# Performance work log

Measured on AMD Instinct MI355X. Metric: run time of the kernel, lower is better.

The kernel has to match this reference:

```python
import jax, jax.numpy as jnp
import numpy as np

D_MODEL = 512
NUM_HEADS = 8
D_K = D_MODEL // NUM_HEADS


def setup_inputs() -> dict:
    key = jax.random.key(0)
    ks = jax.random.split(key, 11)
    B, S = 2, 4096
    s = 1.0 / np.sqrt(D_MODEL)
    inp = {
        "q": jax.random.normal(ks[0], (B, S, D_MODEL), jnp.float32),
        "k": jax.random.normal(ks[1], (B, S, D_MODEL), jnp.float32),
        "v": jax.random.normal(ks[2], (B, S, D_MODEL), jnp.float32),
        "W_q": jax.random.normal(ks[3], (D_MODEL, D_MODEL), jnp.float32) * s,
        "b_q": jnp.zeros((D_MODEL,), jnp.float32),
        "W_k": jax.random.normal(ks[4], (D_MODEL, D_MODEL), jnp.float32) * s,
        "b_k": jnp.zeros((D_MODEL,), jnp.float32),
        "W_v": jax.random.normal(ks[5], (D_MODEL, D_MODEL), jnp.float32) * s,
        "b_v": jnp.zeros((D_MODEL,), jnp.float32),
        "W_o": jax.random.normal(ks[6], (D_MODEL, D_MODEL), jnp.float32) * s,
        "b_o": jnp.zeros((D_MODEL,), jnp.float32),
    }
    return inp


def reference(q, k, v, W_q, b_q, W_k, b_k, W_v, b_v, W_o, b_o):
    B, S, _ = q.shape

    def proj(x, W, b):
        # Linear then split heads: [B,S,D] -> [B,H,S,d_k]
        y = x @ W.T + b
        return y.reshape(B, S, NUM_HEADS, D_K).transpose(0, 2, 1, 3)

    Q = proj(q, W_q, b_q)
    K = proj(k, W_k, b_k)
    V = proj(v, W_v, b_v)
    scores = jnp.einsum("bhsd,bhtd->bhst", Q, K) / jnp.sqrt(jnp.float32(D_K))
    attn = jax.nn.softmax(scores, axis=-1)  # dropout=0.0 -> identity
    ctx = jnp.einsum("bhst,bhtd->bhsd", attn, V)
    ctx = ctx.transpose(0, 2, 1, 3).reshape(B, S, D_MODEL)
    return ctx @ W_o.T + b_o
```

## Files before the change

kernel.cpp:

```cpp
#include <hip/hip_runtime.h>


#define DM   512
#define NH   8
#define DK   64
#define SEQ  4096
#define BATCH 2
#define MROWS (BATCH*SEQ)
#define KVT  128
#define CSC  0.18033688011112042f
#define MBIAS 12.0f

typedef __attribute__((ext_vector_type(4))) float  f32x4;
typedef __attribute__((ext_vector_type(8))) short  s16x8;
typedef __attribute__((ext_vector_type(4))) short  s16x4;
typedef __attribute__((ext_vector_type(4))) unsigned short u16x4;
typedef __attribute__((ext_vector_type(4))) int    i32x4;
typedef __attribute__((ext_vector_type(2))) int    i32x2;

static __device__ __forceinline__ unsigned short f2bf(float f) {
    union { float f; unsigned int u; } a; a.f = f;
    unsigned int r = a.u + 0x7FFFu + ((a.u >> 16) & 1u);
    return (unsigned short)(r >> 16);
}
static __device__ __forceinline__ int cvtpk(float lo, float hi) {
    int r;
    asm("v_cvt_pk_bf16_f32 %0, %1, %2" : "=v"(r) : "v"(lo), "v"(hi));
    return r;
}
static __device__ __forceinline__ float fexp2(float x) {
    float r;
    asm("v_exp_f32 %0, %1" : "=v"(r) : "v"(x));
    return r;
}
static __device__ __forceinline__ void swap32(int &a, int &b) {
    auto t = __builtin_amdgcn_permlane32_swap(a, b, false, false);
    a = t[0]; b = t[1];
}
static __device__ __forceinline__ void swap16(int &a, int &b) {
    auto t = __builtin_amdgcn_permlane16_swap(a, b, false, false);
    a = t[0]; b = t[1];
}

__global__ __launch_bounds__(256)
void convert_w(const float* __restrict__ W0, const float* __restrict__ W1,
               const float* __restrict__ W2, const float* __restrict__ W3,
               unsigned short* __restrict__ O)
{
    const int idx   = blockIdx.x * 256 + threadIdx.x;
    const int which = idx >> 15;
    const int off   = (idx & 32767) * 8;
    const float* W = (which == 0) ? W0 : (which == 1) ? W1 : (which == 2) ? W2 : W3;
    f32x4 a = *(const f32x4*)(W + off);
    f32x4 b = *(const f32x4*)(W + off + 4);
    i32x4 pk;
    pk[0] = cvtpk(a[0], a[1]); pk[1] = cvtpk(a[2], a[3]);
    pk[2] = cvtpk(b[0], b[1]); pk[3] = cvtpk(b[2], b[3]);
    *(i32x4*)(O + (size_t)which * (DM * DM) + off) = pk;
}

__global__ __launch_bounds__(256)
void gemm_proj3(const float* __restrict__ a0, const float* __restrict__ a1,
                const float* __restrict__ a2,
                const unsigned short* __restrict__ Wb,
                const float* __restrict__ b0, const float* __restrict__ b1,
                const float* __restrict__ b2,
                unsigned short* __restrict__ O0, unsigned short* __restrict__ O1,
                unsigned short* __restrict__ O2)
{
    __shared__ short As[128 * 40];
    __shared__ short Bs[128 * 40];

    const int z = blockIdx.z;
    const float* A   = (z == 0) ? a0 : (z == 1) ? a1 : a2;
    const short* W   = (const short*)Wb + (size_t)z * DM * DM;
    const float* bias= (z == 0) ? b0 : (z == 1) ? b1 : b2;
    unsigned short* O= (z == 0) ? O0 : (z == 1) ? O1 : O2;
    const float oscale = (z == 0) ? CSC : 1.0f;
    const bool  vt = (z == 2);

    const int tid  = threadIdx.x;
    const int lane = tid & 63;
    const int wid  = tid >> 6;
    const int g = lane >> 4, r = lane & 15;
    const int wm = wid >> 1, wn = wid & 1;
    const int brow = blockIdx.x * 128;
    const int bcol = blockIdx.y * 128;

    f32x4 acc[4][4];
    #pragma unroll
    for (int i = 0; i < 4; ++i)
        #pragma unroll
        for (int j = 0; j < 4; ++j) acc[i][j] = (f32x4)(0.0f);

    for (int k0 = 0; k0 < DM; k0 += 32) {
        #pragma unroll
        for (int j = 0; j < 4; ++j) {
            int c = tid + 256 * j;
            int row = c >> 3, cc = c & 7;
            f32x4 v = *(const f32x4*)(A + (size_t)(brow + row) * DM + k0 + cc * 4);
            i32x2 pk;
            pk[0] = cvtpk(v[0], v[1]);
            pk[1] = cvtpk(v[2], v[3]);
            *(i32x2*)(&As[row * 40 + cc * 4]) = pk;
        }
        #pragma unroll
        for (int j = 0; j < 2; ++j) {
            int c = tid + 256 * j;
            int row = c >> 2, cc = c & 3;
            s16x8 v = *(const s16x8*)(W + (size_t)(bcol + row) * DM + k0 + cc * 8);
            *(s16x8*)(&Bs[row * 40 + cc * 8]) = v;
        }
        __syncthreads();

        s16x8 af[4], bfr[4];
        #pragma unroll
        for (int mf = 0; mf < 4; ++mf)
            af[mf] = *(const s16x8*)(&As[(wm * 64 + mf * 16 + r) * 40 + g * 8]);
        #pragma unroll
        for (int nf = 0; nf < 4; ++nf)
            bfr[nf] = *(const s16x8*)(&Bs[(wn * 64 + nf * 16 + r) * 40 + g * 8]);
        #pragma unroll
        for (int mf = 0; mf < 4; ++mf)
            #pragma unroll
            for (int nf = 0; nf < 4; ++nf)
                acc[mf][nf] = __builtin_amdgcn_mfma_f32_16x16x32_bf16(
                    af[mf], bfr[nf], acc[mf][nf], 0, 0, 0);
        __syncthreads();
    }

    const int ncolbase = bcol + wn * 64;
    const int mrowbase = brow + wm * 64;
    #pragma unroll
    for (int mf = 0; mf < 4; ++mf) {
        #pragma unroll
        for (int nf = 0; nf < 4; ++nf) {
            const int ncol = ncolbase + nf * 16 + r;
            const int m0   = mrowbase + mf * 16 + g * 4;
            const float bv = bias[ncol];
            const int h = ncol >> 6, d = ncol & 63;
            if (!vt) {
                #pragma unroll
                for (int i = 0; i < 4; ++i) {
                    int m = m0 + i;
                    int b = m >> 12, s = m & (SEQ - 1);
                    O[((size_t)(b * NH + h) * SEQ + s) * DK + d] =
                        f2bf((acc[mf][nf][i] + bv) * oscale);
                }
            } else {
                const int b = m0 >> 12, s0 = m0 & (SEQ - 1);
                u16x4 pk;
                #pragma unroll
                for (int i = 0; i < 4; ++i) pk[i] = f2bf(acc[mf][nf][i] + bv);
                *(u16x4*)(&O[((size_t)(b * NH + h) * DK + d) * SEQ + s0]) = pk;
            }
        }
    }
}

__global__ __launch_bounds__(256)
void gemm_out(const unsigned short* __restrict__ Ctx,
              const unsigned short* __restrict__ Wb,
              const float* __restrict__ bias,
              float* __restrict__ O)
{
    __shared__ short As[64 * 40];
    __shared__ short Bs[128 * 40];

    const int tid  = threadIdx.x;
    const int lane = tid & 63;
    const int wid  = tid >> 6;
    const int g = lane >> 4, r = lane & 15;
    const int wm = wid >> 1, wn = wid & 1;
    const int brow = blockIdx.x * 64;
    const int bcol = blockIdx.y * 128;
    const short* W = (const short*)Wb;

    f32x4 acc[2][4];
    #pragma unroll
    for (int i = 0; i < 2; ++i)
        #pragma unroll
        for (int j = 0; j < 4; ++j) acc[i][j] = (f32x4)(0.0f);

    for (int k0 = 0; k0 < DM; k0 += 32) {
        {
            int row = tid >> 2, cc = tid & 3;
            s16x8 v = *(const s16x8*)((const short*)Ctx +
                        (size_t)(brow + row) * DM + k0 + cc * 8);
            *(s16x8*)(&As[row * 40 + cc * 8]) = v;
        }
        #pragma unroll
        for (int j = 0; j < 2; ++j) {
            int c = tid + 256 * j;
            int row = c >> 2, cc = c & 3;
            s16x8 v = *(const s16x8*)(W + (size_t)(bcol + row) * DM + k0 + cc * 8);
            *(s16x8*)(&Bs[row * 40 + cc * 8]) = v;
        }
        __syncthreads();

        s16x8 af[2], bfr[4];
        #pragma unroll
        for (int mf = 0; mf < 2; ++mf)
            af[mf] = *(const s16x8*)(&As[(wm * 32 + mf * 16 + r) * 40 + g * 8]);
        #pragma unroll
        for (int nf = 0; nf < 4; ++nf)
            bfr[nf] = *(const s16x8*)(&Bs[(wn * 64 + nf * 16 + r) * 40 + g * 8]);
        #pragma unroll
        for (int mf = 0; mf < 2; ++mf)
            #pragma unroll
            for (int nf = 0; nf < 4; ++nf)
                acc[mf][nf] = __builtin_amdgcn_mfma_f32_16x16x32_bf16(
                    af[mf], bfr[nf], acc[mf][nf], 0, 0, 0);
        __syncthreads();
    }

    const int ncolbase = bcol + wn * 64;
    const int mrowbase = brow + wm * 32;
    #pragma unroll
    for (int mf = 0; mf < 2; ++mf) {
        #pragma unroll
        for (int nf = 0; nf < 4; ++nf) {
            const int ncol = ncolbase + nf * 16 + r;
            const int m0   = mrowbase + mf * 16 + g * 4;
            const float bv = bias[ncol];
            #pragma unroll
            for (int i = 0; i < 4; ++i)
                O[(size_t)(m0 + i) * DM + ncol] = acc[mf][nf][i] + bv;
        }
    }
}

__global__ __launch_bounds__(512, 4)
void attn_kernel(const unsigned short* __restrict__ Qw,
                 const unsigned short* __restrict__ Kw,
                 const unsigned short* __restrict__ Vtw,
                 unsigned short* __restrict__ Ctx)
{
    __shared__ short Kbuf[2][KVT * 64];
    __shared__ short Vbuf[2][64 * KVT];

    const int tid  = threadIdx.x;
    const int lane = tid & 63;
    const int wid  = tid >> 6;
    const int g = lane >> 4, r = lane & 15;

    const int B   = blockIdx.x;
    const int xcd = B & 7;
    const int j   = B >> 3;
    const int bh  = xcd * 2 + (j >> 5);
    const int qt  = j & 31;
    const int q0  = qt * 128 + wid * 16;

    const short* Qp = (const short*)Qw  + (size_t)bh * SEQ * DK;
    const short* Kp = (const short*)Kw  + (size_t)bh * SEQ * DK;
    const short* Vp = (const short*)Vtw + (size_t)bh * DK * SEQ;

    s16x8 qfr[2];
    #pragma unroll
    for (int df = 0; df < 2; ++df)
        qfr[df] = *(const s16x8*)(Qp + (size_t)(q0 + r) * DK + df * 32 + g * 8);

    s16x8 ones;
    #pragma unroll
    for (int i = 0; i < 8; ++i) ones[i] = (short)0x3F80;

    f32x4 o[4];
    #pragma unroll
    for (int df = 0; df < 4; ++df) o[df] = (f32x4)(0.0f);
    f32x4 l_acc = (f32x4)(0.0f);

    int    lwk[2], lwv[2];
    size_t kgo[2], vgo[2];
    #pragma unroll
    for (int jj = 0; jj < 2; ++jj) {
        int c = tid + 512 * jj;
        int krow = c >> 3, kcc = c & 7;
        kgo[jj] = (size_t)krow * DK + kcc * 8;
        lwk[jj] = krow * 64 + ((kcc ^ (krow & 7)) * 8);
        int vrow = c >> 4, vcc = c & 15;
        vgo[jj] = (size_t)vrow * SEQ + vcc * 8;
        lwv[jj] = vrow * KVT + ((vcc ^ (vrow & 15)) * 8);
    }

    s16x8 kr[2], vr[2];
    #pragma unroll
    for (int jj = 0; jj < 2; ++jj) {
        kr[jj] = *(const s16x8*)(Kp + kgo[jj]);
        vr[jj] = *(const s16x8*)(Vp + vgo[jj]);
    }

    int cur = 0;
    for (int t0 = 0; t0 < SEQ; t0 += KVT) {
        short* kb = Kbuf[cur];
        short* vb = Vbuf[cur];
        #pragma unroll
        for (int jj = 0; jj < 2; ++jj) {
            *(s16x8*)(&kb[lwk[jj]]) = kr[jj];
            *(s16x8*)(&vb[lwv[jj]]) = vr[jj];
        }
        if (t0 + KVT < SEQ) {
            #pragma unroll
            for (int jj = 0; jj < 2; ++jj) {
                kr[jj] = *(const s16x8*)(Kp + (size_t)(t0 + KVT) * DK + kgo[jj]);
                vr[jj] = *(const s16x8*)(Vp + vgo[jj] + t0 + KVT);
            }
        }
        asm volatile("s_waitcnt lgkmcnt(0)\n\ts_barrier" ::: "memory");
        __builtin_amdgcn_sched_barrier(0);

        f32x4 s[8];
        #pragma unroll
        for (int tf = 0; tf < 8; ++tf) s[tf] = (f32x4)(-MBIAS);
        __builtin_amdgcn_s_setprio(1);
        #pragma unroll
        for (int tf = 0; tf < 8; ++tf) {
            const short* krow = &kb[(tf * 16 + r) * 64];
            s16x8 ka0 = *(const s16x8*)(krow + ((g ^ (r & 7)) * 8));
            s16x8 ka1 = *(const s16x8*)(krow + (((4 | g) ^ (r & 7)) * 8));
            s[tf] = __builtin_amdgcn_mfma_f32_16x16x32_bf16(ka0, qfr[0], s[tf], 0, 0, 0);
            s[tf] = __builtin_amdgcn_mfma_f32_16x16x32_bf16(ka1, qfr[1], s[tf], 0, 0, 0);
        }
        __builtin_amdgcn_s_setprio(0);

        #pragma unroll
        for (int tf = 0; tf < 8; ++tf) {
            s[tf][0] = fexp2(s[tf][0]);
            s[tf][1] = fexp2(s[tf][1]);
            s[tf][2] = fexp2(s[tf][2]);
            s[tf][3] = fexp2(s[tf][3]);
        }

        s16x8 pb[4];
        #pragma unroll
        for (int h = 0; h < 4; ++h) {
            int A0 = cvtpk(s[2 * h][0],     s[2 * h][1]);
            int A1 = cvtpk(s[2 * h][2],     s[2 * h][3]);
            int A2 = cvtpk(s[2 * h + 1][0], s[2 * h + 1][1]);
            int A3 = cvtpk(s[2 * h + 1][2], s[2 * h + 1][3]);
            swap32(A0, A2); swap16(A0, A2);
            swap32(A1, A3); swap16(A1, A3);
            i32x4 w; w[0] = A0; w[1] = A1; w[2] = A2; w[3] = A3;
            pb[h] = __builtin_bit_cast(s16x8, w);
        }

        __builtin_amdgcn_s_setprio(1);
        #pragma unroll
        for (int h = 0; h < 4; ++h)
            l_acc = __builtin_amdgcn_mfma_f32_16x16x32_bf16(ones, pb[h], l_acc, 0, 0, 0);
        #pragma unroll
        for (int df = 0; df < 4; ++df) {
            const short* vrow = &vb[(df * 16 + r) * KVT];
            #pragma unroll
            for (int h = 0; h < 4; ++h) {
                s16x8 va = *(const s16x8*)(vrow + (((h * 4 + g) ^ r) * 8));
                o[df] = __builtin_amdgcn_mfma_f32_16x16x32_bf16(va, pb[h], o[df], 0, 0, 0);
            }
        }
        __builtin_amdgcn_s_setprio(0);

        cur ^= 1;
    }

    const int b = bh >> 3, h2 = bh & 7;
    {
        const float inv = 1.0f / l_acc[0];
        const int q = q0 + r;
        const size_t rowoff = (size_t)(b * SEQ + q) * DM + h2 * DK;
        #pragma unroll
        for (int df = 0; df < 4; ++df) {
            u16x4 pk;
            #pragma unroll
            for (int i = 0; i < 4; ++i) pk[i] = f2bf(o[df][i] * inv);
            *(u16x4*)(&Ctx[rowoff + df * 16 + g * 4]) = pk;
        }
    }
}

extern "C" void kernel_launch(void* const* d_in, const int* in_sizes, int n_in,
                              void* d_out, int out_size, void* d_ws, size_t ws_size,
                              hipStream_t stream)
{
    const float* q  = (const float*)d_in[0];
    const float* k  = (const float*)d_in[1];
    const float* v  = (const float*)d_in[2];
    const float* Wq = (const float*)d_in[3];
    const float* bq = (const float*)d_in[4];
    const float* Wk = (const float*)d_in[5];
    const float* bk = (const float*)d_in[6];
    const float* Wv = (const float*)d_in[7];
    const float* bv = (const float*)d_in[8];
    const float* Wo = (const float*)d_in[9];
    const float* bo = (const float*)d_in[10];

    const size_t NE = (size_t)MROWS * DM;
    unsigned short* ws  = (unsigned short*)d_ws;
    unsigned short* Qw  = ws;
    unsigned short* Kw  = Qw  + NE;
    unsigned short* Vtw = Kw  + NE;
    unsigned short* Ctx = Vtw + NE;
    unsigned short* Wb  = Ctx + NE;

    convert_w<<<512, 256, 0, stream>>>(Wq, Wk, Wv, Wo, Wb);
    dim3 gg3(MROWS / 128, DM / 128, 3);
    gemm_proj3<<<gg3, 256, 0, stream>>>(q, k, v, Wb, bq, bk, bv, Qw, Kw, Vtw);
    attn_kernel<<<512, 512, 0, stream>>>(Qw, Kw, Vtw, Ctx);
    dim3 ggo(MROWS / 64, DM / 128);
    gemm_out<<<ggo, 256, 0, stream>>>(Ctx, Wb + (size_t)3 * DM * DM, bo, (float*)d_out);
}
```

Before: 137.0 us.

## Double-buffer LDS and register-prefetch global loads in projection GEMMs

Both projection GEMM kernels now use two LDS buffers and prefetch the next K-tile from global memory into registers while the current tile is computed. The trailing barrier of each iteration is dropped, leaving one barrier per iteration with a manual lgkmcnt wait. This is meant to hide global load latency behind MFMA work and halve barrier count, at the cost of doubled LDS use and more registers, which may lower occupancy.

```diff
diff --git a/kernel.cpp b/kernel.cpp
--- a/kernel.cpp
+++ b/kernel.cpp
@@ -68,8 +68,8 @@
                 unsigned short* __restrict__ O0, unsigned short* __restrict__ O1,
                 unsigned short* __restrict__ O2)
 {
-    __shared__ short As[128 * 40];
-    __shared__ short Bs[128 * 40];
+    __shared__ short As[2][128 * 40];
+    __shared__ short Bs[2][128 * 40];
 
     const int z = blockIdx.z;
     const float* A   = (z == 0) ? a0 : (z == 1) ? a1 : a2;
@@ -87,46 +87,71 @@
     const int brow = blockIdx.x * 128;
     const int bcol = blockIdx.y * 128;
 
+    const float* agp[4]; int alw[4];
+    #pragma unroll
+    for (int j = 0; j < 4; ++j) {
+        int c = tid + 256 * j;
+        int row = c >> 3, cc = c & 7;
+        agp[j] = A + (size_t)(brow + row) * DM + cc * 4;
+        alw[j] = row * 40 + cc * 4;
+    }
+    const short* wgp[2]; int wlw[2];
+    #pragma unroll
+    for (int j = 0; j < 2; ++j) {
+        int c = tid + 256 * j;
+        int row = c >> 2, cc = c & 3;
+        wgp[j] = W + (size_t)(bcol + row) * DM + cc * 8;
+        wlw[j] = row * 40 + cc * 8;
+    }
+
     f32x4 acc[4][4];
     #pragma unroll
     for (int i = 0; i < 4; ++i)
         #pragma unroll
         for (int j = 0; j < 4; ++j) acc[i][j] = (f32x4)(0.0f);
 
+    f32x4 ar[4]; s16x8 wr[2];
+    #pragma unroll
+    for (int j = 0; j < 4; ++j) ar[j] = *(const f32x4*)(agp[j]);
+    #pragma unroll
+    for (int j = 0; j < 2; ++j) wr[j] = *(const s16x8*)(wgp[j]);
+
+    int cur = 0;
     for (int k0 = 0; k0 < DM; k0 += 32) {
+        short* as = As[cur];
+        short* bs = Bs[cur];
         #pragma unroll
         for (int j = 0; j < 4; ++j) {
-            int c = tid + 256 * j;
-            int row = c >> 3, cc = c & 7;
-            f32x4 v = *(const f32x4*)(A + (size_t)(brow + row) * DM + k0 + cc * 4);
             i32x2 pk;
-            pk[0] = cvtpk(v[0], v[1]);
-            pk[1] = cvtpk(v[2], v[3]);
-            *(i32x2*)(&As[row * 40 + cc * 4]) = pk;
-        }
-        #pragma unroll
-        for (int j = 0; j < 2; ++j) {
-            int c = tid + 256 * j;
-            int row = c >> 2, cc = c & 3;
-            s16x8 v = *(const s16x8*)(W + (size_t)(bcol + row) * DM + k0 + cc * 8);
-            *(s16x8*)(&Bs[row * 40 + cc * 8]) = v;
-        }
-        __syncthreads();
+            pk[0] = cvtpk(ar[j][0], ar[j][1]);
+            pk[1] = cvtpk(ar[j][2], ar[j][3]);
+            *(i32x2*)(&as[alw[j]]) = pk;
+        }
+        #pragma unroll
+        for (int j = 0; j < 2; ++j) *(s16x8*)(&bs[wlw[j]]) = wr[j];
+        if (k0 + 32 < DM) {
+            #pragma unroll
+            for (int j = 0; j < 4; ++j) ar[j] = *(const f32x4*)(agp[j] + k0 + 32);
+            #pragma unroll
+            for (int j = 0; j < 2; ++j) wr[j] = *(const s16x8*)(wgp[j] + k0 + 32);
+        }
+        asm volatile("s_waitcnt lgkmcnt(0)\n\ts_barrier" ::: "memory");
+        __builtin_amdgcn_sched_barrier(0);
 
         s16x8 af[4], bfr[4];
         #pragma unroll
         for (int mf = 0; mf < 4; ++mf)
-            af[mf] = *(const s16x8*)(&As[(wm * 64 + mf * 16 + r) * 40 + g * 8]);
+            af[mf] = *(const s16x8*)(&as[(wm * 64 + mf * 16 + r) * 40 + g * 8]);
         #pragma unroll
         for (int nf = 0; nf < 4; ++nf)
-            bfr[nf] = *(const s16x8*)(&Bs[(wn * 64 + nf * 16 + r) * 40 + g * 8]);
+            bfr[nf] = *(const s16x8*)(&bs[(wn * 64 + nf * 16 + r) * 40 + g * 8]);
         #pragma unroll
         for (int mf = 0; mf < 4; ++mf)
             #pragma unroll
             for (int nf = 0; nf < 4; ++nf)
                 acc[mf][nf] = __builtin_amdgcn_mfma_f32_16x16x32_bf16(
                     af[mf], bfr[nf], acc[mf][nf], 0, 0, 0);
-        __syncthreads();
+        cur ^= 1;
     }
 
     const int ncolbase = bcol + wn * 64;
@@ -164,8 +189,8 @@
               const float* __restrict__ bias,
               float* __restrict__ O)
 {
-    __shared__ short As[64 * 40];
-    __shared__ short Bs[128 * 40];
+    __shared__ short As[2][64 * 40];
+    __shared__ short Bs[2][128 * 40];
 
     const int tid  = threadIdx.x;
     const int lane = tid & 63;
@@ -176,42 +201,61 @@
     const int bcol = blockIdx.y * 128;
     const short* W = (const short*)Wb;
 
+    const short* agp; int alw;
+    {
+        int row = tid >> 2, cc = tid & 3;
+        agp = (const short*)Ctx + (size_t)(brow + row) * DM + cc * 8;
+        alw = row * 40 + cc * 8;
+    }
+    const short* wgp[2]; int wlw[2];
+    #pragma unroll
+    for (int j = 0; j < 2; ++j) {
+        int c = tid + 256 * j;
+        int row = c >> 2, cc = c & 3;
+        wgp[j] = W + (size_t)(bcol + row) * DM + cc * 8;
+        wlw[j] = row * 40 + cc * 8;
+    }
+
     f32x4 acc[2][4];
     #pragma unroll
     for (int i = 0; i < 2; ++i)
         #pragma unroll
         for (int j = 0; j < 4; ++j) acc[i][j] = (f32x4)(0.0f);
 
+    s16x8 ar; s16x8 wr[2];
+    ar = *(const s16x8*)agp;
+    #pragma unroll
+    for (int j = 0; j < 2; ++j) wr[j] = *(const s16x8*)(wgp[j]);
+
+    int cur = 0;
     for (int k0 = 0; k0 < DM; k0 += 32) {
-        {
-            int row = tid >> 2, cc = tid & 3;
-            s16x8 v = *(const s16x8*)((const short*)Ctx +
-                        (size_t)(brow + row) * DM + k0 + cc * 8);
-            *(s16x8*)(&As[row * 40 + cc * 8]) = v;
-        }
-        #pragma unroll
-        for (int j = 0; j < 2; ++j) {
-            int c = tid + 256 * j;
-            int row = c >> 2, cc = c & 3;
-            s16x8 v = *(const s16x8*)(W + (size_t)(bcol + row) * DM + k0 + cc * 8);
-            *(s16x8*)(&Bs[row * 40 + cc * 8]) = v;
-        }
-        __syncthreads();
+        short* as = As[cur];
+        short* bs = Bs[cur];
+        *(s16x8*)(&as[alw]) = ar;
+        #pragma unroll
+        for (int j = 0; j < 2; ++j) *(s16x8*)(&bs[wlw[j]]) = wr[j];
+        if (k0 + 32 < DM) {
+            ar = *(const s16x8*)(agp + k0 + 32);
+            #pragma unroll
+            for (int j = 0; j < 2; ++j) wr[j] = *(const s16x8*)(wgp[j] + k0 + 32);
+        }
+        asm volatile("s_waitcnt lgkmcnt(0)\n\ts_barrier" ::: "memory");
+        __builtin_amdgcn_sched_barrier(0);
 
         s16x8 af[2], bfr[4];
         #pragma unroll
         for (int mf = 0; mf < 2; ++mf)
-            af[mf] = *(const s16x8*)(&As[(wm * 32 + mf * 16 + r) * 40 + g * 8]);
+            af[mf] = *(const s16x8*)(&as[(wm * 32 + mf * 16 + r) * 40 + g * 8]);
         #pragma unroll
         for (int nf = 0; nf < 4; ++nf)
-            bfr[nf] = *(const s16x8*)(&Bs[(wn * 64 + nf * 16 + r) * 40 + g * 8]);
+            bfr[nf] = *(const s16x8*)(&bs[(wn * 64 + nf * 16 + r) * 40 + g * 8]);
         #pragma unroll
         for (int mf = 0; mf < 2; ++mf)
             #pragma unroll
             for (int nf = 0; nf < 4; ++nf)
                 acc[mf][nf] = __builtin_amdgcn_mfma_f32_16x16x32_bf16(
                     af[mf], bfr[nf], acc[mf][nf], 0, 0, 0);
-        __syncthreads();
+        cur ^= 1;
     }
 
     const int ncolbase = bcol + wn * 64;
```

Result: faster. 124.1 us (median of 2 runs) (-9.4%).
